# Optimization experiments

Measured on AMD Instinct MI355X. Metric: run time of the kernel, lower is better.

Reference implementation:

```python
import jax, jax.numpy as jnp
import numpy as np

B, L, S, D, H = 32, 256, 64, 128, 4
DH = D // H
EPS = 1e-5


def _uniform(k, shape, scale):
    return jax.random.uniform(k, shape, jnp.float32, -scale, scale)


def setup_inputs() -> dict:
    key = jax.random.key(0)
    ks = jax.random.split(key, 12)
    sc = 1.0 / np.sqrt(D)
    return {
        "h_wq": jax.random.normal(ks[0], (B, L, D), jnp.float32),
        "h_all": jax.random.normal(ks[1], (B, L, S, D), jnp.float32),
        "station_id": jax.random.randint(ks[2], (B,), 0, S),
        "adj": jax.random.randint(ks[3], (S, S), 0, 2).astype(jnp.float32),
        "in_proj_w": _uniform(ks[4], (3 * D, D), sc),
        "in_proj_b": _uniform(ks[5], (3 * D,), sc),
        "out_w": _uniform(ks[6], (D, D), sc),
        "out_b": _uniform(ks[7], (D,), sc),
        "gate_w": _uniform(ks[8], (D, 2 * D), 1.0 / np.sqrt(2 * D)),
        "gate_b": _uniform(ks[9], (D,), 1.0 / np.sqrt(2 * D)),
        "ln_g": jnp.ones((D,), jnp.float32),
        "ln_b": jnp.zeros((D,), jnp.float32),
        "alpha": jnp.asarray(0.1, jnp.float32),
    }


def _allowed_mask(adj, station_id):
    # allowed[b, s] == True  <=> station s may attend as key for sample b
    sid = station_id.astype(jnp.int32)
    allowed = adj[sid] > 0.0                                  # [B, S]
    self_oh = jax.nn.one_hot(sid, adj.shape[0], dtype=bool)   # [B, S]
    allowed = allowed & ~self_oh                              # exclude self
    # fallback-to-all for rows with no neighbor (still excluding self)
    no_nb = ~jnp.any(allowed, axis=1, keepdims=True)
    allowed = jnp.where(no_nb, ~self_oh, allowed)
    # final safety: if STILL empty (S==1 edge case), allow self
    no_nb2 = ~jnp.any(allowed, axis=1, keepdims=True)
    allowed = allowed | (no_nb2 & self_oh)
    return allowed


def _forward(h_wq, h_all, station_id, adj, in_proj_w, in_proj_b,
             out_w, out_b, gate_w, gate_b, ln_g, ln_b, alpha):
    b, l, d = h_wq.shape
    s = h_all.shape[2]
    qw, kw, vw = jnp.split(in_proj_w, 3, axis=0)
    qb, kb, vb = jnp.split(in_proj_b, 3, axis=0)

    q = (h_wq @ qw.T + qb).reshape(b, l, H, DH)        # [B,L,H,DH]
    k = (h_all @ kw.T + kb).reshape(b, l, s, H, DH)    # [B,L,S,H,DH]
    v = (h_all @ vw.T + vb).reshape(b, l, s, H, DH)

    scores = jnp.einsum('blhd,blshd->blhs', q, k) / np.sqrt(DH)  # [B,L,H,S]
    allowed = _allowed_mask(adj, station_id)                     # [B,S]
    scores = jnp.where(allowed[:, None, None, :], scores, -jnp.inf)
    w = jax.nn.softmax(scores, axis=-1)

    ctx = jnp.einsum('blhs,blshd->blhd', w, v).reshape(b, l, d)
    ctx = ctx @ out_w.T + out_b                                  # out_proj

    g = jax.nn.sigmoid(jnp.concatenate([h_wq, ctx], axis=-1) @ gate_w.T + gate_b)
    y = h_wq + alpha * (g * ctx)                                 # dropout = eval mode

    mu = jnp.mean(y, axis=-1, keepdims=True)
    var = jnp.mean(jnp.square(y - mu), axis=-1, keepdims=True)
    return (y - mu) * jax.lax.rsqrt(var + EPS) * ln_g + ln_b


def reference(h_wq, h_all, station_id, adj, in_proj_w, in_proj_b,
              out_w, out_b, gate_w, gate_b, ln_g, ln_b, alpha):
    return _forward(h_wq, h_all, station_id, adj, in_proj_w, in_proj_b,
                    out_w, out_b, gate_w, gate_b, ln_g, ln_b, alpha)
```

## Files before the change

### kernel.cpp

```cpp
#include <hip/hip_runtime.h>
#include <math.h>

#define B_   32
#define L_   256
#define S_   64
#define D_   128
#define H_   4
#define DH_  32
#define NTOK (B_*L_)

#define QK_OFF   0
#define QK_BYTES ((size_t)NTOK*512*4)
#define CB_OFF   (QK_OFF + QK_BYTES)
#define CB_BYTES ((size_t)NTOK*4*4)
#define CTX_OFF  (CB_OFF + CB_BYTES)

__global__ __launch_bounds__(256) void qk_kernel(
        const float* __restrict__ h_wq,
        const float* __restrict__ in_proj_w, const float* __restrict__ in_proj_b,
        float* __restrict__ qk_out, float* __restrict__ cb_out) {
    __shared__ float x_lds[32*128];
    __shared__ float q_lds[32*128];
    const int t0 = blockIdx.x * 32;
    const int tid = threadIdx.x;

    {
        const float4* src = (const float4*)(h_wq + (size_t)t0*128);
        float4* dst = (float4*)x_lds;
        for (int e = tid; e < 32*32; e += 256) dst[e] = src[e];
    }
    __syncthreads();

    const int d = tid & 127, half = tid >> 7;
    const float* xb = x_lds + half*16*128;
    {
        float acc[16];
        const float qb = in_proj_b[d];
        #pragma unroll
        for (int t = 0; t < 16; ++t) acc[t] = qb;
        const float4* wrow = (const float4*)(in_proj_w + (size_t)d*128);
        for (int j4 = 0; j4 < 32; ++j4) {
            float4 w = wrow[j4];
            #pragma unroll
            for (int t = 0; t < 16; ++t) {
                float4 x = *(const float4*)(xb + t*128 + j4*4);
                acc[t] += w.x*x.x + w.y*x.y + w.z*x.z + w.w*x.w;
            }
        }
        #pragma unroll
        for (int t = 0; t < 16; ++t) q_lds[(half*16+t)*128 + d] = acc[t];
    }
    __syncthreads();

    const float scale = 0.17677669529663687f;
    const float* qbse = q_lds + half*16*128;
    #pragma unroll
    for (int h = 0; h < 4; ++h) {
        float acc[16];
        #pragma unroll
        for (int t = 0; t < 16; ++t) acc[t] = 0.f;
        for (int j = 0; j < 32; ++j) {
            float w = in_proj_w[(size_t)(128 + h*32 + j)*128 + d];
            #pragma unroll
            for (int t = 0; t < 16; ++t) acc[t] += w * qbse[t*128 + h*32 + j];
        }
        #pragma unroll
        for (int t = 0; t < 16; ++t)
            qk_out[(size_t)(t0 + half*16 + t)*512 + h*128 + d] = acc[t] * scale;
    }
    if (tid < 128) {
        int t = tid >> 2, h = tid & 3;
        float s = 0.f;
        for (int j = 0; j < 32; ++j)
            s += q_lds[t*128 + h*32 + j] * in_proj_b[128 + h*32 + j];
        cb_out[(t0 + t)*4 + h] = s * scale;
    }
}

__global__ __launch_bounds__(256) void attn_kernel(
        const float* __restrict__ h_all,
        const float* __restrict__ in_proj_w, const float* __restrict__ in_proj_b,
        const float* __restrict__ qk_buf, const float* __restrict__ cb_buf,
        const int* __restrict__ station_id, const float* __restrict__ adj,
        float* __restrict__ ctx_out) {
    __shared__ float u_lds[4][4*132];
    __shared__ int   lst[64];
    __shared__ int   cnt_s;

    const int t0  = blockIdx.x * 4;
    const int b   = t0 >> 8;
    const int tid = threadIdx.x;
    const int wv  = tid >> 6;
    const int lane = tid & 63;
    const int t = t0 + wv;

    if (tid < 64) {
        int sid = station_id[b];
        int s = tid;
        bool av = (adj[sid*S_ + s] > 0.0f) && (s != sid);
        unsigned long long m = __ballot(av);
        if (m == 0ull) { av = (s != sid); m = __ballot(av); }
        if (m == 0ull) { av = (s == sid); m = __ballot(av); }
        int idx = __popcll(m & ((1ull << s) - 1ull));
        if (av) lst[idx] = s;
        if (s == 0) cnt_s = __popcll(m);
    }

    const float* qkt = qk_buf + (size_t)t*512 + 2*lane;
    const float2 qk0 = *(const float2*)(qkt);
    const float2 qk1 = *(const float2*)(qkt + 128);
    const float2 qk2 = *(const float2*)(qkt + 256);
    const float2 qk3 = *(const float2*)(qkt + 384);
    const float cb0 = cb_buf[t*4+0], cb1 = cb_buf[t*4+1];
    const float cb2 = cb_buf[t*4+2], cb3 = cb_buf[t*4+3];

    __syncthreads();
    const int cnt = cnt_s;
    const float* rowbase = h_all + (size_t)t * (S_*D_) + 2*lane;

    float m0 = -INFINITY, m1 = -INFINITY, m2 = -INFINITY, m3 = -INFINITY;
    float l0 = 0.f, l1 = 0.f, l2 = 0.f, l3 = 0.f;
    float2 u0 = {0.f,0.f}, u1 = {0.f,0.f}, u2 = {0.f,0.f}, u3 = {0.f,0.f};

    for (int i = 0; i < cnt; ++i) {
        float2 x = *(const float2*)(rowbase + lst[i]*D_);
        float p0 = qk0.x*x.x + qk0.y*x.y;
        float p1 = qk1.x*x.x + qk1.y*x.y;
        float p2 = qk2.x*x.x + qk2.y*x.y;
        float p3 = qk3.x*x.x + qk3.y*x.y;
        #pragma unroll
        for (int o = 32; o >= 1; o >>= 1) {
            p0 += __shfl_xor(p0, o);
            p1 += __shfl_xor(p1, o);
            p2 += __shfl_xor(p2, o);
            p3 += __shfl_xor(p3, o);
        }
        float s0 = p0 + cb0, s1 = p1 + cb1, s2 = p2 + cb2, s3 = p3 + cb3;
        float n0 = fmaxf(m0, s0), r0 = __expf(m0 - n0), w0 = __expf(s0 - n0);
        l0 = l0*r0 + w0; u0.x = u0.x*r0 + w0*x.x; u0.y = u0.y*r0 + w0*x.y; m0 = n0;
        float n1 = fmaxf(m1, s1), r1 = __expf(m1 - n1), w1 = __expf(s1 - n1);
        l1 = l1*r1 + w1; u1.x = u1.x*r1 + w1*x.x; u1.y = u1.y*r1 + w1*x.y; m1 = n1;
        float n2 = fmaxf(m2, s2), r2 = __expf(m2 - n2), w2 = __expf(s2 - n2);
        l2 = l2*r2 + w2; u2.x = u2.x*r2 + w2*x.x; u2.y = u2.y*r2 + w2*x.y; m2 = n2;
        float n3 = fmaxf(m3, s3), r3 = __expf(m3 - n3), w3 = __expf(s3 - n3);
        l3 = l3*r3 + w3; u3.x = u3.x*r3 + w3*x.x; u3.y = u3.y*r3 + w3*x.y; m3 = n3;
    }
    {
        float i0 = 1.f/l0, i1 = 1.f/l1, i2 = 1.f/l2, i3 = 1.f/l3;
        u0.x *= i0; u0.y *= i0;  u1.x *= i1; u1.y *= i1;
        u2.x *= i2; u2.y *= i2;  u3.x *= i3; u3.y *= i3;
        *(float2*)&u_lds[wv][0*132 + 2*lane] = u0;
        *(float2*)&u_lds[wv][1*132 + 2*lane] = u1;
        *(float2*)&u_lds[wv][2*132 + 2*lane] = u2;
        *(float2*)&u_lds[wv][3*132 + 2*lane] = u3;
    }
    __syncthreads();

    if (tid < 128) {
        const int d = tid, h = d >> 5;
        const float4* vwrow = (const float4*)(in_proj_w + (size_t)(256 + d)*128);
        const float vb = in_proj_b[256 + d];
        float a0 = vb, a1 = vb, a2 = vb, a3 = vb;
        #pragma unroll 8
        for (int j4 = 0; j4 < 32; ++j4) {
            float4 w = vwrow[j4];
            float4 v0 = *(const float4*)(&u_lds[0][h*132 + j4*4]);
            float4 v1 = *(const float4*)(&u_lds[1][h*132 + j4*4]);
            float4 v2 = *(const float4*)(&u_lds[2][h*132 + j4*4]);
            float4 v3 = *(const float4*)(&u_lds[3][h*132 + j4*4]);
            a0 += w.x*v0.x + w.y*v0.y + w.z*v0.z + w.w*v0.w;
            a1 += w.x*v1.x + w.y*v1.y + w.z*v1.z + w.w*v1.w;
            a2 += w.x*v2.x + w.y*v2.y + w.z*v2.z + w.w*v2.w;
            a3 += w.x*v3.x + w.y*v3.y + w.z*v3.z + w.w*v3.w;
        }
        ctx_out[(size_t)(t0+0)*128 + d] = a0;
        ctx_out[(size_t)(t0+1)*128 + d] = a1;
        ctx_out[(size_t)(t0+2)*128 + d] = a2;
        ctx_out[(size_t)(t0+3)*128 + d] = a3;
    }
}

__global__ __launch_bounds__(256) void epi_kernel(
        const float* __restrict__ h_wq, const float* __restrict__ ctx_buf,
        const float* __restrict__ out_w, const float* __restrict__ out_b,
        const float* __restrict__ gate_w, const float* __restrict__ gate_b,
        const float* __restrict__ ln_g, const float* __restrict__ ln_b,
        const float* __restrict__ alpha, float* __restrict__ out) {
    __shared__ float c_tile[32*128];
    __shared__ float x_tile[32*128];
    __shared__ float o_tile[32*128];
    __shared__ float mu_s[32], rs_s[32];
    const int t0 = blockIdx.x * 32;
    const int tid = threadIdx.x;

    {
        const float4* cs = (const float4*)(ctx_buf + (size_t)t0*128);
        const float4* xs = (const float4*)(h_wq + (size_t)t0*128);
        float4* cd = (float4*)c_tile; float4* xd = (float4*)x_tile;
        for (int e = tid; e < 32*32; e += 256) { cd[e] = cs[e]; xd[e] = xs[e]; }
    }
    __syncthreads();

    const int d = tid & 127, half = tid >> 7;
    float o_acc[16];
    {
        const float ob = out_b[d];
        #pragma unroll
        for (int t = 0; t < 16; ++t) o_acc[t] = ob;
        const float4* wrow = (const float4*)(out_w + (size_t)d*128);
        const float* cbp = c_tile + half*16*128;
        for (int j4 = 0; j4 < 32; ++j4) {
            float4 w = wrow[j4];
            #pragma unroll
            for (int t = 0; t < 16; ++t) {
                float4 c = *(const float4*)(cbp + t*128 + j4*4);
                o_acc[t] += w.x*c.x + w.y*c.y + w.z*c.z + w.w*c.w;
            }
        }
        #pragma unroll
        for (int t = 0; t < 16; ++t) o_tile[(half*16+t)*128 + d] = o_acc[t];
    }
    __syncthreads();

    {
        float g_acc[16];
        const float gb = gate_b[d];
        #pragma unroll
        for (int t = 0; t < 16; ++t) g_acc[t] = gb;
        const float4* wrow = (const float4*)(gate_w + (size_t)d*256);
        const float* xb = x_tile + half*16*128;
        const float* obp = o_tile + half*16*128;
        for (int j4 = 0; j4 < 32; ++j4) {
            float4 w0 = wrow[j4];
            float4 w1 = wrow[32 + j4];
            #pragma unroll
            for (int t = 0; t < 16; ++t) {
                float4 x = *(const float4*)(xb  + t*128 + j4*4);
                float4 o = *(const float4*)(obp + t*128 + j4*4);
                g_acc[t] += w0.x*x.x + w0.y*x.y + w0.z*x.z + w0.w*x.w
                          + w1.x*o.x + w1.y*o.y + w1.z*o.z + w1.w*o.w;
            }
        }
        const float al = alpha[0];
        #pragma unroll
        for (int t = 0; t < 16; ++t) {
            float g = 1.0f / (1.0f + __expf(-g_acc[t]));
            float y = xb[t*128 + d] + al * g * o_acc[t];
            c_tile[(half*16+t)*128 + d] = y;
        }
    }
    __syncthreads();

    {
        int tt = tid >> 3, k = tid & 7;
        const float* yr = c_tile + tt*128;
        float s = 0.f;
        for (int dd = k; dd < 128; dd += 8) s += yr[dd];
        for (int o = 4; o >= 1; o >>= 1) s += __shfl_xor(s, o, 8);
        float mu = s * (1.0f/128.0f);
        float vs = 0.f;
        for (int dd = k; dd < 128; dd += 8) { float df = yr[dd] - mu; vs += df*df; }
        for (int o = 4; o >= 1; o >>= 1) vs += __shfl_xor(vs, o, 8);
        if (k == 0) { mu_s[tt] = mu; rs_s[tt] = rsqrtf(vs*(1.0f/128.0f) + 1e-5f); }
    }
    __syncthreads();

    for (int e = tid; e < 32*128; e += 256) {
        int tt = e >> 7, dd = e & 127;
        float y = c_tile[e];
        out[(size_t)t0*128 + e] = (y - mu_s[tt]) * rs_s[tt] * ln_g[dd] + ln_b[dd];
    }
}

extern "C" void kernel_launch(void* const* d_in, const int* in_sizes, int n_in,
                              void* d_out, int out_size, void* d_ws, size_t ws_size,
                              hipStream_t stream) {
    const float* h_wq       = (const float*)d_in[0];
    const float* h_all      = (const float*)d_in[1];
    const int*   station_id = (const int*)  d_in[2];
    const float* adj        = (const float*)d_in[3];
    const float* in_proj_w  = (const float*)d_in[4];
    const float* in_proj_b  = (const float*)d_in[5];
    const float* out_w      = (const float*)d_in[6];
    const float* out_b      = (const float*)d_in[7];
    const float* gate_w     = (const float*)d_in[8];
    const float* gate_b     = (const float*)d_in[9];
    const float* ln_g       = (const float*)d_in[10];
    const float* ln_b       = (const float*)d_in[11];
    const float* alpha      = (const float*)d_in[12];

    char* ws = (char*)d_ws;
    float* qk   = (float*)(ws + QK_OFF);
    float* cb   = (float*)(ws + CB_OFF);
    float* ctx  = (float*)(ws + CTX_OFF);
    float* out  = (float*)d_out;

    qk_kernel  <<<NTOK/32, 256, 0, stream>>>(h_wq, in_proj_w, in_proj_b, qk, cb);
    attn_kernel<<<NTOK/4, 256, 0, stream>>>(h_all, in_proj_w, in_proj_b, qk, cb,
                                            station_id, adj, ctx);
    epi_kernel <<<NTOK/32, 256, 0, stream>>>(h_wq, ctx, out_w, out_b, gate_w,
                                             gate_b, ln_g, ln_b, alpha, out);
}
```

Measured before the change: 471.3 us.

## Split attention wave into per-head 16-lane groups and use all threads for V projection

Each wave's 64 lanes are now split into four 16-lane groups, one per head. Each lane loads 8 contiguous floats of the gathered station row with float4 loads and reduces the score with a 4-step shuffle inside its group, instead of every lane handling all four heads with 6-step full-wave reductions. The online softmax now runs once per lane instead of four times. The V-projection epilogue uses all 256 threads, two tokens each, instead of 128 threads doing four tokens. This cuts shuffle and exp work per gathered row and makes each lane's loads wider; each group also keeps its own running max and sum.

```diff
diff --git a/kernel.cpp b/kernel.cpp
--- a/kernel.cpp
+++ b/kernel.cpp
@@ -92,6 +92,8 @@
     const int tid = threadIdx.x;
     const int wv  = tid >> 6;
     const int lane = tid & 63;
+    const int g   = lane >> 4;
+    const int lg  = lane & 15;
     const int t = t0 + wv;
 
     if (tid < 64) {
@@ -106,77 +108,65 @@
         if (s == 0) cnt_s = __popcll(m);
     }
 
-    const float* qkt = qk_buf + (size_t)t*512 + 2*lane;
-    const float2 qk0 = *(const float2*)(qkt);
-    const float2 qk1 = *(const float2*)(qkt + 128);
-    const float2 qk2 = *(const float2*)(qkt + 256);
-    const float2 qk3 = *(const float2*)(qkt + 384);
-    const float cb0 = cb_buf[t*4+0], cb1 = cb_buf[t*4+1];
-    const float cb2 = cb_buf[t*4+2], cb3 = cb_buf[t*4+3];
+    const float* qkp = qk_buf + (size_t)t*512 + g*128 + 8*lg;
+    const float4 qa = *(const float4*)(qkp);
+    const float4 qb = *(const float4*)(qkp + 4);
+    const float cbg = cb_buf[t*4 + g];
 
     __syncthreads();
     const int cnt = cnt_s;
-    const float* rowbase = h_all + (size_t)t * (S_*D_) + 2*lane;
-
-    float m0 = -INFINITY, m1 = -INFINITY, m2 = -INFINITY, m3 = -INFINITY;
-    float l0 = 0.f, l1 = 0.f, l2 = 0.f, l3 = 0.f;
-    float2 u0 = {0.f,0.f}, u1 = {0.f,0.f}, u2 = {0.f,0.f}, u3 = {0.f,0.f};
-
+    const float* rowbase = h_all + (size_t)t * (S_*D_) + 8*lg;
+
+    float mg = -INFINITY, lsum = 0.f;
+    float4 ua = {0.f,0.f,0.f,0.f}, ub = {0.f,0.f,0.f,0.f};
+
+    #pragma unroll 2
     for (int i = 0; i < cnt; ++i) {
-        float2 x = *(const float2*)(rowbase + lst[i]*D_);
-        float p0 = qk0.x*x.x + qk0.y*x.y;
-        float p1 = qk1.x*x.x + qk1.y*x.y;
-        float p2 = qk2.x*x.x + qk2.y*x.y;
-        float p3 = qk3.x*x.x + qk3.y*x.y;
-        #pragma unroll
-        for (int o = 32; o >= 1; o >>= 1) {
-            p0 += __shfl_xor(p0, o);
-            p1 += __shfl_xor(p1, o);
-            p2 += __shfl_xor(p2, o);
-            p3 += __shfl_xor(p3, o);
-        }
-        float s0 = p0 + cb0, s1 = p1 + cb1, s2 = p2 + cb2, s3 = p3 + cb3;
-        float n0 = fmaxf(m0, s0), r0 = __expf(m0 - n0), w0 = __expf(s0 - n0);
-        l0 = l0*r0 + w0; u0.x = u0.x*r0 + w0*x.x; u0.y = u0.y*r0 + w0*x.y; m0 = n0;
-        float n1 = fmaxf(m1, s1), r1 = __expf(m1 - n1), w1 = __expf(s1 - n1);
-        l1 = l1*r1 + w1; u1.x = u1.x*r1 + w1*x.x; u1.y = u1.y*r1 + w1*x.y; m1 = n1;
-        float n2 = fmaxf(m2, s2), r2 = __expf(m2 - n2), w2 = __expf(s2 - n2);
-        l2 = l2*r2 + w2; u2.x = u2.x*r2 + w2*x.x; u2.y = u2.y*r2 + w2*x.y; m2 = n2;
-        float n3 = fmaxf(m3, s3), r3 = __expf(m3 - n3), w3 = __expf(s3 - n3);
-        l3 = l3*r3 + w3; u3.x = u3.x*r3 + w3*x.x; u3.y = u3.y*r3 + w3*x.y; m3 = n3;
-    }
-    {
-        float i0 = 1.f/l0, i1 = 1.f/l1, i2 = 1.f/l2, i3 = 1.f/l3;
-        u0.x *= i0; u0.y *= i0;  u1.x *= i1; u1.y *= i1;
-        u2.x *= i2; u2.y *= i2;  u3.x *= i3; u3.y *= i3;
-        *(float2*)&u_lds[wv][0*132 + 2*lane] = u0;
-        *(float2*)&u_lds[wv][1*132 + 2*lane] = u1;
-        *(float2*)&u_lds[wv][2*132 + 2*lane] = u2;
-        *(float2*)&u_lds[wv][3*132 + 2*lane] = u3;
-    }
-    __syncthreads();
-
-    if (tid < 128) {
-        const int d = tid, h = d >> 5;
+        const float* rp = rowbase + lst[i]*D_;
+        float4 xa = *(const float4*)(rp);
+        float4 xb = *(const float4*)(rp + 4);
+        float p = qa.x*xa.x + qa.y*xa.y + qa.z*xa.z + qa.w*xa.w
+                + qb.x*xb.x + qb.y*xb.y + qb.z*xb.z + qb.w*xb.w;
+        p += __shfl_xor(p, 8, 16);
+        p += __shfl_xor(p, 4, 16);
+        p += __shfl_xor(p, 2, 16);
+        p += __shfl_xor(p, 1, 16);
+        float s = p + cbg;
+        float n = fmaxf(mg, s);
+        float r = __expf(mg - n), w = __expf(s - n);
+        lsum = lsum*r + w;
+        ua.x = ua.x*r + w*xa.x; ua.y = ua.y*r + w*xa.y;
+        ua.z = ua.z*r + w*xa.z; ua.w = ua.w*r + w*xa.w;
+        ub.x = ub.x*r + w*xb.x; ub.y = ub.y*r + w*xb.y;
+        ub.z = ub.z*r + w*xb.z; ub.w = ub.w*r + w*xb.w;
+        mg = n;
+    }
+    {
+        float inv = 1.f / lsum;
+        ua.x *= inv; ua.y *= inv; ua.z *= inv; ua.w *= inv;
+        ub.x *= inv; ub.y *= inv; ub.z *= inv; ub.w *= inv;
+        *(float4*)&u_lds[wv][g*132 + 8*lg]     = ua;
+        *(float4*)&u_lds[wv][g*132 + 8*lg + 4] = ub;
+    }
+    __syncthreads();
+
+    {
+        const int d = tid & 127, pr = tid >> 7, h = (tid & 127) >> 5;
         const float4* vwrow = (const float4*)(in_proj_w + (size_t)(256 + d)*128);
         const float vb = in_proj_b[256 + d];
-        float a0 = vb, a1 = vb, a2 = vb, a3 = vb;
+        float a0 = vb, a1 = vb;
+        const float* uA = &u_lds[2*pr][h*132];
+        const float* uB = &u_lds[2*pr+1][h*132];
         #pragma unroll 8
         for (int j4 = 0; j4 < 32; ++j4) {
             float4 w = vwrow[j4];
-            float4 v0 = *(const float4*)(&u_lds[0][h*132 + j4*4]);
-            float4 v1 = *(const float4*)(&u_lds[1][h*132 + j4*4]);
-            float4 v2 = *(const float4*)(&u_lds[2][h*132 + j4*4]);
-            float4 v3 = *(const float4*)(&u_lds[3][h*132 + j4*4]);
+            float4 v0 = *(const float4*)(uA + j4*4);
+            float4 v1 = *(const float4*)(uB + j4*4);
             a0 += w.x*v0.x + w.y*v0.y + w.z*v0.z + w.w*v0.w;
             a1 += w.x*v1.x + w.y*v1.y + w.z*v1.z + w.w*v1.w;
-            a2 += w.x*v2.x + w.y*v2.y + w.z*v2.z + w.w*v2.w;
-            a3 += w.x*v3.x + w.y*v3.y + w.z*v3.z + w.w*v3.w;
-        }
-        ctx_out[(size_t)(t0+0)*128 + d] = a0;
-        ctx_out[(size_t)(t0+1)*128 + d] = a1;
-        ctx_out[(size_t)(t0+2)*128 + d] = a2;
-        ctx_out[(size_t)(t0+3)*128 + d] = a3;
+        }
+        ctx_out[(size_t)(t0 + 2*pr    )*128 + d] = a0;
+        ctx_out[(size_t)(t0 + 2*pr + 1)*128 + d] = a1;
     }
 }
 
```

Result: no change. 466.3 us (-1.1%).
